# Kernel tuning notes

Measured on AMD Instinct MI355X. Metric: run time of the kernel, lower is better.

## Reference

```python
import jax, jax.numpy as jnp
import numpy as np

N_NODES = 100000
LEAKY_SLOPE = 0.01  # nn.LeakyReLU default

def setup_inputs() -> dict:
    key = jax.random.key(0)
    k1, k2, k3, k4, k5, k6 = jax.random.split(key, 6)
    in_dim, out_dim, ef_dim = 64, 64, 32
    E = 500000
    nf = jax.random.normal(k1, (N_NODES, in_dim), dtype=jnp.float32)
    ef = jax.random.normal(k2, (E, ef_dim), dtype=jnp.float32)
    src = jax.random.randint(k3, (E,), 0, N_NODES, dtype=jnp.int64 if jax.config.jax_enable_x64 else jnp.int32)
    dst = jax.random.randint(k4, (E,), 0, N_NODES, dtype=src.dtype)
    # torch Linear weights: (out, in), no bias
    We = jax.random.normal(k5, (out_dim, 2 * in_dim + ef_dim), dtype=jnp.float32) * 0.05
    Wn = jax.random.normal(k6, (out_dim, out_dim + in_dim), dtype=jnp.float32) * 0.05
    return {"nf": nf, "ef": ef, "src": src, "dst": dst, "We": We, "Wn": Wn}

def reference(nf, ef, src, dst, We, Wn):
    # Module adds reverse edges sharing the same edge features
    src_all = jnp.concatenate([src, dst])          # [2E]
    dst_all = jnp.concatenate([dst, src])          # [2E]
    ef_all = jnp.concatenate([ef, ef], axis=0)     # [2E, ef_dim]
    # message: concat(src_nf, dst_nf, ef) -> Linear -> LeakyReLU
    m_in = jnp.concatenate([nf[src_all], nf[dst_all], ef_all], axis=-1)  # [2E, 2*in+ef]
    msg = jax.nn.leaky_relu(m_in @ We.T, negative_slope=LEAKY_SLOPE)     # [2E, out]
    # reduce: sum messages at destination nodes
    red = jax.ops.segment_sum(msg, dst_all, num_segments=N_NODES)       # [N, out]
    # apply: concat(nf, red_msg) -> Linear -> LeakyReLU
    n_in = jnp.concatenate([nf, red], axis=-1)                          # [N, in+out]
    out_nf = jax.nn.leaky_relu(n_in @ Wn.T, negative_slope=LEAKY_SLOPE)
    return out_nf
```

## Files before the change

### kernel.cpp

```cpp
#include <hip/hip_runtime.h>
#include <stdint.h>


#define LEAKY(x) fmaxf((x), 0.01f * (x))
#define CAP 40
#define SCAT_BLOCKS 2048
typedef _Float16 f16;
typedef _Float16 h2 __attribute__((ext_vector_type(2)));
typedef int iv4 __attribute__((ext_vector_type(4)));

static __device__ __forceinline__ int swz(int k, int c) {
    return k * 128 + (c ^ (((k >> 2) & 7) << 2));
}

union H4 { f16 h[4]; h2 p[2]; short4 s; long long ll; };
union H8 { f16 h[8]; h2 p[4]; int4 q; };

__global__ void prep_weights_kernel(const float* __restrict__ We,
                                    const float* __restrict__ Wn,
                                    float* __restrict__ WTab,
                                    float* __restrict__ WTc,
                                    float* __restrict__ WTn,
                                    int* __restrict__ cnt, int N)
{
    const int stride = gridDim.x * blockDim.x;
    int i = blockIdx.x * blockDim.x + threadIdx.x;
    for (int j = i; j < 8192 + 2048 + 8192; j += stride) {
        if (j < 8192) {
            int k = j >> 7, n = j & 127;
            WTab[j] = We[(n & 63) * 160 + (n >> 6) * 64 + k];
        } else if (j < 10240) {
            int q = j - 8192; int k = q >> 6, n = q & 63;
            WTc[q] = We[n * 160 + 128 + k];
        } else {
            int q = j - 10240; int k = q >> 6, n = q & 63;
            WTn[q] = Wn[n * 128 + k];
        }
    }
    const int C4 = N * 4;
    for (int j = i; j < C4; j += stride) cnt[j] = 0;
}

static __device__ void scatter_body(int vb,
    const int* __restrict__ src, const int* __restrict__ dst,
    int* __restrict__ cnt, int2* __restrict__ inc, int E, int N)
{
    const int part = vb & 7;
    const int lo = (int)(((long long)N * part) >> 3);
    const int hi = (int)(((long long)N * (part + 1)) >> 3);
    const int tid = (vb >> 3) * 256 + threadIdx.x;
    const int tpp = (SCAT_BLOCKS >> 3) * 256;
    const int E4 = E >> 2;
    const iv4* src4 = (const iv4*)src;
    const iv4* dst4 = (const iv4*)dst;
    #define PUT(node, nbr, eid) \
        if ((node) >= lo && (node) < hi) { \
            const int p = atomicAdd(&cnt[(node) * 4], 1); \
            if (p < CAP) inc[(size_t)(node) * CAP + p] = make_int2((nbr) << 7, (eid) << 7); \
        }
    for (int j = tid; j < E4; j += tpp) {
        const iv4 s = __builtin_nontemporal_load(&src4[j]);
        const iv4 d = __builtin_nontemporal_load(&dst4[j]);
        const int e0 = 4 * j;
        PUT(d.x, s.x, e0 + 0)
        PUT(d.y, s.y, e0 + 1)
        PUT(d.z, s.z, e0 + 2)
        PUT(d.w, s.w, e0 + 3)
        PUT(s.x, d.x, e0 + 0)
        PUT(s.y, d.y, e0 + 1)
        PUT(s.z, d.z, e0 + 2)
        PUT(s.w, d.w, e0 + 3)
    }
    for (int i = (E4 << 2) + tid; i < E; i += tpp) {
        const int s = src[i], d = dst[i];
        PUT(d, s, i)
        PUT(s, d, i)
    }
    #undef PUT
}

static __device__ void gemm_c_body(float* lds, int bid,
    const float4* __restrict__ ef4, const float* __restrict__ WT,
    f16* __restrict__ C16, int M)
{
    float* As = lds;
    float* Ws = lds + 4096;
    const int t = threadIdx.x;
    const int tr = t >> 4, tc = t & 15;
    const int m0 = bid * 128;

    #pragma unroll
    for (int i = 0; i < 2; ++i)
        ((float4*)Ws)[t + 256 * i] = ((const float4*)WT)[t + 256 * i];
    #pragma unroll
    for (int i = 0; i < 4; ++i) {
        const int idx = t + 256 * i;
        const int m = idx >> 3, kq = idx & 7;
        float4 v = make_float4(0.f, 0.f, 0.f, 0.f);
        if (m0 + m < M) v = ef4[(size_t)(m0 + m) * 8 + kq];
        As[swz(4 * kq + 0, m)] = v.x;
        As[swz(4 * kq + 1, m)] = v.y;
        As[swz(4 * kq + 2, m)] = v.z;
        As[swz(4 * kq + 3, m)] = v.w;
    }
    __syncthreads();

    float acc[8][4];
    #pragma unroll
    for (int ri = 0; ri < 8; ++ri)
        #pragma unroll
        for (int ci = 0; ci < 4; ++ci) acc[ri][ci] = 0.f;

    #pragma unroll 8
    for (int k = 0; k < 32; ++k) {
        const float4 aLo = *(const float4*)&As[swz(k, tr * 4)];
        const float4 aHi = *(const float4*)&As[swz(k, 64 + tr * 4)];
        const float4 w  = *(const float4*)&Ws[k * 64 + tc * 4];
        const float av[8] = {aLo.x, aLo.y, aLo.z, aLo.w, aHi.x, aHi.y, aHi.z, aHi.w};
        const float bv[4] = {w.x, w.y, w.z, w.w};
        #pragma unroll
        for (int ri = 0; ri < 8; ++ri)
            #pragma unroll
            for (int ci = 0; ci < 4; ++ci) acc[ri][ci] += av[ri] * bv[ci];
    }

    #pragma unroll
    for (int ri = 0; ri < 8; ++ri) {
        const int v = m0 + ((ri < 4) ? (tr * 4 + ri) : (64 + tr * 4 + ri - 4));
        if (v < M) {
            H4 u;
            #pragma unroll
            for (int j = 0; j < 4; ++j) u.h[j] = (f16)acc[ri][j];
            *(short4*)&C16[(size_t)v * 64 + tc * 4] = u.s;
        }
    }
}

__global__ __launch_bounds__(256) void mega1_kernel(
    const int* __restrict__ src, const int* __restrict__ dst,
    int* __restrict__ cnt, int2* __restrict__ inc,
    const float4* __restrict__ ef4, const float* __restrict__ WTc,
    f16* __restrict__ C16, int E, int N)
{
    __shared__ float lds[6144];
    const int b = blockIdx.x;
    if (b < SCAT_BLOCKS) scatter_body(b, src, dst, cnt, inc, E, N);
    else                 gemm_c_body(lds, b - SCAT_BLOCKS, ef4, WTc, C16, E);
}

__global__ __launch_bounds__(256) void gemm_abp_kernel(
    const float4* __restrict__ nf4, const float* __restrict__ WTab,
    const float* __restrict__ WTn,
    f16* __restrict__ A16, f16* __restrict__ B16, f16* __restrict__ P16, int M)
{
    __shared__ float As[64 * 128];
    __shared__ float Wab[64 * 128];
    __shared__ float Wp[64 * 64];
    const int t = threadIdx.x;
    const int tr = t >> 4, tc = t & 15;
    const int m0 = blockIdx.x * 128;

    #pragma unroll
    for (int i = 0; i < 8; ++i)
        ((float4*)Wab)[t + 256 * i] = ((const float4*)WTab)[t + 256 * i];
    #pragma unroll
    for (int i = 0; i < 4; ++i)
        ((float4*)Wp)[t + 256 * i] = ((const float4*)WTn)[t + 256 * i];
    #pragma unroll
    for (int i = 0; i < 8; ++i) {
        const int idx = t + 256 * i;
        const int m = idx >> 4, kq = idx & 15;
        float4 v = make_float4(0.f, 0.f, 0.f, 0.f);
        if (m0 + m < M) v = nf4[(size_t)(m0 + m) * 16 + kq];
        As[swz(4 * kq + 0, m)] = v.x;
        As[swz(4 * kq + 1, m)] = v.y;
        As[swz(4 * kq + 2, m)] = v.z;
        As[swz(4 * kq + 3, m)] = v.w;
    }
    __syncthreads();

    float acc[8][8];
    float accp[8][4];
    #pragma unroll
    for (int ri = 0; ri < 8; ++ri) {
        #pragma unroll
        for (int ci = 0; ci < 8; ++ci) acc[ri][ci] = 0.f;
        #pragma unroll
        for (int ci = 0; ci < 4; ++ci) accp[ri][ci] = 0.f;
    }

    #pragma unroll 4
    for (int k = 0; k < 64; ++k) {
        const float4 aLo = *(const float4*)&As[swz(k, tr * 4)];
        const float4 aHi = *(const float4*)&As[swz(k, 64 + tr * 4)];
        const float4 bLo = *(const float4*)&Wab[k * 128 + tc * 4];
        const float4 bHi = *(const float4*)&Wab[k * 128 + 64 + tc * 4];
        const float4 w  = *(const float4*)&Wp[k * 64 + tc * 4];
        const float av[8] = {aLo.x, aLo.y, aLo.z, aLo.w, aHi.x, aHi.y, aHi.z, aHi.w};
        const float bv[8] = {bLo.x, bLo.y, bLo.z, bLo.w, bHi.x, bHi.y, bHi.z, bHi.w};
        const float wv[4] = {w.x, w.y, w.z, w.w};
        #pragma unroll
        for (int ri = 0; ri < 8; ++ri) {
            #pragma unroll
            for (int ci = 0; ci < 8; ++ci) acc[ri][ci] += av[ri] * bv[ci];
            #pragma unroll
            for (int ci = 0; ci < 4; ++ci) accp[ri][ci] += av[ri] * wv[ci];
        }
    }

    #pragma unroll
    for (int ri = 0; ri < 8; ++ri) {
        const int v = m0 + ((ri < 4) ? (tr * 4 + ri) : (64 + tr * 4 + ri - 4));
        if (v < M) {
            H4 lo, hi, pu;
            #pragma unroll
            for (int j = 0; j < 4; ++j) {
                lo.h[j] = (f16)acc[ri][j];
                hi.h[j] = (f16)acc[ri][4 + j];
                pu.h[j] = (f16)accp[ri][j];
            }
            *(short4*)&A16[(size_t)v * 64 + tc * 4] = lo.s;
            *(short4*)&B16[(size_t)v * 64 + tc * 4] = hi.s;
            *(short4*)&P16[(size_t)v * 64 + tc * 4] = pu.s;
        }
    }
}

__global__ __launch_bounds__(256, 4) void reduce_kernel(
    const f16* __restrict__ A16, const f16* __restrict__ B16,
    const f16* __restrict__ C16, const int* __restrict__ cnt,
    const int2* __restrict__ inc, f16* __restrict__ red16, int N)
{
    const int lane = threadIdx.x & 63;
    const int g = lane >> 3;
    const int sub = lane & 7;
    const int sub16 = sub * 16;
    const char* Ab = (const char*)A16;
    const char* Cb = (const char*)C16;
    const int part = blockIdx.x & 7;
    const int NO = (N + 7) >> 3;
    const int olo = (int)(((long long)NO * part) >> 3);
    const int ohi = (int)(((long long)NO * (part + 1)) >> 3);
    const int wid = (((blockIdx.x >> 3) * blockDim.x) + threadIdx.x) >> 6;
    const int wstride = ((gridDim.x >> 3) * blockDim.x) >> 6;
    const _Float16 k01 = (_Float16)0.01f;
    const h2 c001 = {k01, k01};
    for (int oct = olo + wid; oct < ohi; oct += wstride) {
        const int v = oct * 8 + g;
        const int vc = (v < N) ? v : (N - 1);
        const int len = min(cnt[vc * 4], CAP);
        const int ebase = vc * CAP;
        H8 bh; bh.q = *(const int4*)&B16[(size_t)vc * 64 + sub * 8];
        const h2 b0 = bh.p[0], b1 = bh.p[1], b2 = bh.p[2], b3 = bh.p[3];
        int mx = (len + 7) >> 3;
        mx = max(mx, __shfl_xor(mx, 8));
        mx = max(mx, __shfl_xor(mx, 16));
        mx = max(mx, __shfl_xor(mx, 32));
        float a0 = 0.f, a1 = 0.f, a2 = 0.f, a3 = 0.f;
        float a4 = 0.f, a5 = 0.f, a6 = 0.f, a7 = 0.f;
        for (int it = 0; it < mx; ++it) {
            const int el = it * 8;
            const int4 q0 = *(const int4*)&inc[ebase + el];
            const int4 q1 = *(const int4*)&inc[ebase + el + 2];
            const int4 q2 = *(const int4*)&inc[ebase + el + 4];
            const int4 q3 = *(const int4*)&inc[ebase + el + 6];
            float okf[8];
            unsigned ao[8], co[8];
            #pragma unroll
            for (int k2 = 0; k2 < 8; ++k2)
                okf[k2] = ((unsigned)(el + k2) < (unsigned)len) ? 1.0f : 0.0f;
            const int qa[8] = {q0.x, q0.z, q1.x, q1.z, q2.x, q2.z, q3.x, q3.z};
            const int qc[8] = {q0.y, q0.w, q1.y, q1.w, q2.y, q2.w, q3.y, q3.w};
            #pragma unroll
            for (int k2 = 0; k2 < 8; ++k2) {
                ao[k2] = (okf[k2] != 0.0f) ? (unsigned)qa[k2] : 0u;
                co[k2] = (okf[k2] != 0.0f) ? (unsigned)qc[k2] : 0u;
            }
            H8 Av[8], Cv[8];
            #pragma unroll
            for (int k2 = 0; k2 < 8; ++k2) {
                Av[k2].q = *(const int4*)(Ab + (size_t)ao[k2] + sub16);
                Cv[k2].q = *(const int4*)(Cb + (size_t)co[k2] + sub16);
            }
            #pragma unroll
            for (int k2 = 0; k2 < 8; ++k2) {
                h2 s0 = Av[k2].p[0] + Cv[k2].p[0] + b0;
                h2 s1 = Av[k2].p[1] + Cv[k2].p[1] + b1;
                h2 s2 = Av[k2].p[2] + Cv[k2].p[2] + b2;
                h2 s3 = Av[k2].p[3] + Cv[k2].p[3] + b3;
                s0 = __builtin_elementwise_max(s0, s0 * c001);
                s1 = __builtin_elementwise_max(s1, s1 * c001);
                s2 = __builtin_elementwise_max(s2, s2 * c001);
                s3 = __builtin_elementwise_max(s3, s3 * c001);
                a0 = fmaf((float)s0[0], okf[k2], a0);
                a1 = fmaf((float)s0[1], okf[k2], a1);
                a2 = fmaf((float)s1[0], okf[k2], a2);
                a3 = fmaf((float)s1[1], okf[k2], a3);
                a4 = fmaf((float)s2[0], okf[k2], a4);
                a5 = fmaf((float)s2[1], okf[k2], a5);
                a6 = fmaf((float)s3[0], okf[k2], a6);
                a7 = fmaf((float)s3[1], okf[k2], a7);
            }
        }
        if (v < N) {
            H8 u;
            u.h[0] = (f16)a0; u.h[1] = (f16)a1; u.h[2] = (f16)a2; u.h[3] = (f16)a3;
            u.h[4] = (f16)a4; u.h[5] = (f16)a5; u.h[6] = (f16)a6; u.h[7] = (f16)a7;
            *(int4*)&red16[(size_t)v * 64 + sub * 8] = u.q;
        }
    }
}

__global__ __launch_bounds__(256) void apply_lite_kernel(
    const f16* __restrict__ red16, const f16* __restrict__ P16,
    const float* __restrict__ WTn, float* __restrict__ out, int M)
{
    __shared__ float As[64 * 128];
    __shared__ float Ws[64 * 64];
    const int t = threadIdx.x;
    const int tr = t >> 4, tc = t & 15;
    const int m0 = blockIdx.x * 128;
    const float* WT1 = WTn + 4096;

    #pragma unroll
    for (int i = 0; i < 4; ++i)
        ((float4*)Ws)[t + 256 * i] = ((const float4*)WT1)[t + 256 * i];
    #pragma unroll
    for (int i = 0; i < 8; ++i) {
        const int idx = t + 256 * i;
        const int m = idx >> 4, kq = idx & 15;
        H4 v; v.ll = 0;
        if (m0 + m < M) v.s = *(const short4*)&red16[(size_t)(m0 + m) * 64 + kq * 4];
        As[swz(4 * kq + 0, m)] = (float)v.h[0];
        As[swz(4 * kq + 1, m)] = (float)v.h[1];
        As[swz(4 * kq + 2, m)] = (float)v.h[2];
        As[swz(4 * kq + 3, m)] = (float)v.h[3];
    }
    __syncthreads();

    float acc[8][4];
    #pragma unroll
    for (int ri = 0; ri < 8; ++ri)
        #pragma unroll
        for (int ci = 0; ci < 4; ++ci) acc[ri][ci] = 0.f;

    #pragma unroll 8
    for (int k = 0; k < 64; ++k) {
        const float4 aLo = *(const float4*)&As[swz(k, tr * 4)];
        const float4 aHi = *(const float4*)&As[swz(k, 64 + tr * 4)];
        const float4 w  = *(const float4*)&Ws[k * 64 + tc * 4];
        const float av[8] = {aLo.x, aLo.y, aLo.z, aLo.w, aHi.x, aHi.y, aHi.z, aHi.w};
        const float bv[4] = {w.x, w.y, w.z, w.w};
        #pragma unroll
        for (int ri = 0; ri < 8; ++ri)
            #pragma unroll
            for (int ci = 0; ci < 4; ++ci) acc[ri][ci] += av[ri] * bv[ci];
    }

    #pragma unroll
    for (int ri = 0; ri < 8; ++ri) {
        const int v = m0 + ((ri < 4) ? (tr * 4 + ri) : (64 + tr * 4 + ri - 4));
        if (v < M) {
            H4 pv; pv.s = *(const short4*)&P16[(size_t)v * 64 + tc * 4];
            float4 o;
            o.x = LEAKY(acc[ri][0] + (float)pv.h[0]);
            o.y = LEAKY(acc[ri][1] + (float)pv.h[1]);
            o.z = LEAKY(acc[ri][2] + (float)pv.h[2]);
            o.w = LEAKY(acc[ri][3] + (float)pv.h[3]);
            *(float4*)&out[(size_t)v * 64 + tc * 4] = o;
        }
    }
}

extern "C" void kernel_launch(void* const* d_in, const int* in_sizes, int n_in,
                              void* d_out, int out_size, void* d_ws, size_t ws_size,
                              hipStream_t stream) {
    const float* nf  = (const float*)d_in[0];
    const float* ef  = (const float*)d_in[1];
    const int*   src = (const int*)d_in[2];
    const int*   dst = (const int*)d_in[3];
    const float* We  = (const float*)d_in[4];
    const float* Wn  = (const float*)d_in[5];

    const int N = in_sizes[0] / 64;
    const int E = in_sizes[2];

    char* p = (char*)d_ws;
    auto alloc = [&](size_t bytes) -> char* {
        char* r = p; p += (bytes + 255) & ~(size_t)255; return r;
    };
    f16*   red16 = (f16*)alloc((size_t)N * 64 * 2);
    float* WTab  = (float*)alloc(8192 * 4);
    float* WTc   = (float*)alloc(2048 * 4);
    float* WTn   = (float*)alloc(8192 * 4);
    int2*  inc   = (int2*)alloc((size_t)N * CAP * 8);
    int*   cnt   = (int*)alloc((size_t)N * 4 * 4);
    f16*   A16   = (f16*)alloc((size_t)N * 64 * 2);
    f16*   B16   = (f16*)alloc((size_t)N * 64 * 2);
    f16*   C16   = (f16*)alloc((size_t)E * 64 * 2);
    f16*   P16   = (f16*)alloc((size_t)N * 64 * 2);

    const int nC = (E + 127) >> 7;
    const int nAB = (N + 127) >> 7;
    const int NO = (N + 7) >> 3;
    const int redBlocks = (((NO + 3) / 4) + 7) & ~7;

    prep_weights_kernel<<<512, 256, 0, stream>>>(We, Wn, WTab, WTc, WTn, cnt, N);
    mega1_kernel<<<SCAT_BLOCKS + nC, 256, 0, stream>>>(src, dst, cnt, inc,
                                                       (const float4*)ef, WTc, C16, E, N);
    gemm_abp_kernel<<<nAB, 256, 0, stream>>>((const float4*)nf, WTab, WTn,
                                             A16, B16, P16, N);
    reduce_kernel<<<redBlocks, 256, 0, stream>>>(A16, B16, C16, cnt, inc, red16, N);
    apply_lite_kernel<<<(N + 127) / 128, 256, 0, stream>>>(red16, P16, WTn, (float*)d_out, N);
}
```

Measured before the change: 288.6 us.

## Fuse node apply GEMM into reduce kernel and halve scatter blocks

```diff
diff --git a/kernel.cpp b/kernel.cpp
--- a/kernel.cpp
+++ b/kernel.cpp
@@ -4,7 +4,7 @@
 
 #define LEAKY(x) fmaxf((x), 0.01f * (x))
 #define CAP 40
-#define SCAT_BLOCKS 2048
+#define SCAT_BLOCKS 1024
 typedef _Float16 f16;
 typedef _Float16 h2 __attribute__((ext_vector_type(2)));
 typedef int iv4 __attribute__((ext_vector_type(4)));
@@ -229,12 +229,23 @@
 __global__ __launch_bounds__(256, 4) void reduce_kernel(
     const f16* __restrict__ A16, const f16* __restrict__ B16,
     const f16* __restrict__ C16, const int* __restrict__ cnt,
-    const int2* __restrict__ inc, f16* __restrict__ red16, int N)
-{
+    const int2* __restrict__ inc, const f16* __restrict__ P16,
+    const float* __restrict__ WTn, float* __restrict__ outp, int N)
+{
+    __shared__ float W1[64 * 64];
+    {
+        const float4* wsrc = (const float4*)(WTn + 4096);
+        #pragma unroll
+        for (int i = 0; i < 4; ++i)
+            ((float4*)W1)[threadIdx.x + 256 * i] = wsrc[threadIdx.x + 256 * i];
+    }
+    __syncthreads();
+
     const int lane = threadIdx.x & 63;
     const int g = lane >> 3;
     const int sub = lane & 7;
     const int sub16 = sub * 16;
+    const int gbase = lane & 56;
     const char* Ab = (const char*)A16;
     const char* Cb = (const char*)C16;
     const int part = blockIdx.x & 7;
@@ -256,8 +267,7 @@
         mx = max(mx, __shfl_xor(mx, 8));
         mx = max(mx, __shfl_xor(mx, 16));
         mx = max(mx, __shfl_xor(mx, 32));
-        float a0 = 0.f, a1 = 0.f, a2 = 0.f, a3 = 0.f;
-        float a4 = 0.f, a5 = 0.f, a6 = 0.f, a7 = 0.f;
+        float areg[8] = {0.f, 0.f, 0.f, 0.f, 0.f, 0.f, 0.f, 0.f};
         for (int it = 0; it < mx; ++it) {
             const int el = it * 8;
             const int4 q0 = *(const int4*)&inc[ebase + el];
@@ -292,82 +302,44 @@
                 s1 = __builtin_elementwise_max(s1, s1 * c001);
                 s2 = __builtin_elementwise_max(s2, s2 * c001);
                 s3 = __builtin_elementwise_max(s3, s3 * c001);
-                a0 = fmaf((float)s0[0], okf[k2], a0);
-                a1 = fmaf((float)s0[1], okf[k2], a1);
-                a2 = fmaf((float)s1[0], okf[k2], a2);
-                a3 = fmaf((float)s1[1], okf[k2], a3);
-                a4 = fmaf((float)s2[0], okf[k2], a4);
-                a5 = fmaf((float)s2[1], okf[k2], a5);
-                a6 = fmaf((float)s3[0], okf[k2], a6);
-                a7 = fmaf((float)s3[1], okf[k2], a7);
+                areg[0] = fmaf((float)s0[0], okf[k2], areg[0]);
+                areg[1] = fmaf((float)s0[1], okf[k2], areg[1]);
+                areg[2] = fmaf((float)s1[0], okf[k2], areg[2]);
+                areg[3] = fmaf((float)s1[1], okf[k2], areg[3]);
+                areg[4] = fmaf((float)s2[0], okf[k2], areg[4]);
+                areg[5] = fmaf((float)s2[1], okf[k2], areg[5]);
+                areg[6] = fmaf((float)s3[0], okf[k2], areg[6]);
+                areg[7] = fmaf((float)s3[1], okf[k2], areg[7]);
+            }
+        }
+        H8 pv; pv.q = *(const int4*)&P16[(size_t)vc * 64 + sub * 8];
+        float o[8];
+        #pragma unroll
+        for (int j = 0; j < 8; ++j) o[j] = (float)pv.h[j];
+        #pragma unroll
+        for (int r = 0; r < 8; ++r) {
+            const float av = areg[r];
+            #pragma unroll
+            for (int s = 0; s < 8; ++s) {
+                const int k = s * 8 + r;
+                const float rk = __shfl(av, gbase + s, 64);
+                const float4 w0 = *(const float4*)&W1[k * 64 + sub * 8];
+                const float4 w1 = *(const float4*)&W1[k * 64 + sub * 8 + 4];
+                o[0] = fmaf(rk, w0.x, o[0]);
+                o[1] = fmaf(rk, w0.y, o[1]);
+                o[2] = fmaf(rk, w0.z, o[2]);
+                o[3] = fmaf(rk, w0.w, o[3]);
+                o[4] = fmaf(rk, w1.x, o[4]);
+                o[5] = fmaf(rk, w1.y, o[5]);
+                o[6] = fmaf(rk, w1.z, o[6]);
+                o[7] = fmaf(rk, w1.w, o[7]);
             }
         }
         if (v < N) {
-            H8 u;
-            u.h[0] = (f16)a0; u.h[1] = (f16)a1; u.h[2] = (f16)a2; u.h[3] = (f16)a3;
-            u.h[4] = (f16)a4; u.h[5] = (f16)a5; u.h[6] = (f16)a6; u.h[7] = (f16)a7;
-            *(int4*)&red16[(size_t)v * 64 + sub * 8] = u.q;
-        }
-    }
-}
-
-__global__ __launch_bounds__(256) void apply_lite_kernel(
-    const f16* __restrict__ red16, const f16* __restrict__ P16,
-    const float* __restrict__ WTn, float* __restrict__ out, int M)
-{
-    __shared__ float As[64 * 128];
-    __shared__ float Ws[64 * 64];
-    const int t = threadIdx.x;
-    const int tr = t >> 4, tc = t & 15;
-    const int m0 = blockIdx.x * 128;
-    const float* WT1 = WTn + 4096;
-
-    #pragma unroll
-    for (int i = 0; i < 4; ++i)
-        ((float4*)Ws)[t + 256 * i] = ((const float4*)WT1)[t + 256 * i];
-    #pragma unroll
-    for (int i = 0; i < 8; ++i) {
-        const int idx = t + 256 * i;
-        const int m = idx >> 4, kq = idx & 15;
-        H4 v; v.ll = 0;
-        if (m0 + m < M) v.s = *(const short4*)&red16[(size_t)(m0 + m) * 64 + kq * 4];
-        As[swz(4 * kq + 0, m)] = (float)v.h[0];
-        As[swz(4 * kq + 1, m)] = (float)v.h[1];
-        As[swz(4 * kq + 2, m)] = (float)v.h[2];
-        As[swz(4 * kq + 3, m)] = (float)v.h[3];
-    }
-    __syncthreads();
-
-    float acc[8][4];
-    #pragma unroll
-    for (int ri = 0; ri < 8; ++ri)
-        #pragma unroll
-        for (int ci = 0; ci < 4; ++ci) acc[ri][ci] = 0.f;
-
-    #pragma unroll 8
-    for (int k = 0; k < 64; ++k) {
-        const float4 aLo = *(const float4*)&As[swz(k, tr * 4)];
-        const float4 aHi = *(const float4*)&As[swz(k, 64 + tr * 4)];
-        const float4 w  = *(const float4*)&Ws[k * 64 + tc * 4];
-        const float av[8] = {aLo.x, aLo.y, aLo.z, aLo.w, aHi.x, aHi.y, aHi.z, aHi.w};
-        const float bv[4] = {w.x, w.y, w.z, w.w};
-        #pragma unroll
-        for (int ri = 0; ri < 8; ++ri)
-            #pragma unroll
-            for (int ci = 0; ci < 4; ++ci) acc[ri][ci] += av[ri] * bv[ci];
-    }
-
-    #pragma unroll
-    for (int ri = 0; ri < 8; ++ri) {
-        const int v = m0 + ((ri < 4) ? (tr * 4 + ri) : (64 + tr * 4 + ri - 4));
-        if (v < M) {
-            H4 pv; pv.s = *(const short4*)&P16[(size_t)v * 64 + tc * 4];
-            float4 o;
-            o.x = LEAKY(acc[ri][0] + (float)pv.h[0]);
-            o.y = LEAKY(acc[ri][1] + (float)pv.h[1]);
-            o.z = LEAKY(acc[ri][2] + (float)pv.h[2]);
-            o.w = LEAKY(acc[ri][3] + (float)pv.h[3]);
-            *(float4*)&out[(size_t)v * 64 + tc * 4] = o;
+            float4 s0 = make_float4(LEAKY(o[0]), LEAKY(o[1]), LEAKY(o[2]), LEAKY(o[3]));
+            float4 s1 = make_float4(LEAKY(o[4]), LEAKY(o[5]), LEAKY(o[6]), LEAKY(o[7]));
+            *(float4*)&outp[(size_t)v * 64 + sub * 8] = s0;
+            *(float4*)&outp[(size_t)v * 64 + sub * 8 + 4] = s1;
         }
     }
 }
@@ -389,7 +361,6 @@
     auto alloc = [&](size_t bytes) -> char* {
         char* r = p; p += (bytes + 255) & ~(size_t)255; return r;
     };
-    f16*   red16 = (f16*)alloc((size_t)N * 64 * 2);
     float* WTab  = (float*)alloc(8192 * 4);
     float* WTc   = (float*)alloc(2048 * 4);
     float* WTn   = (float*)alloc(8192 * 4);
@@ -410,6 +381,6 @@
                                                        (const float4*)ef, WTc, C16, E, N);
     gemm_abp_kernel<<<nAB, 256, 0, stream>>>((const float4*)nf, WTab, WTn,
                                              A16, B16, P16, N);
-    reduce_kernel<<<redBlocks, 256, 0, stream>>>(A16, B16, C16, cnt, inc, red16, N);
-    apply_lite_kernel<<<(N + 127) / 128, 256, 0, stream>>>(red16, P16, WTn, (float*)d_out, N);
-}
+    reduce_kernel<<<redBlocks, 256, 0, stream>>>(A16, B16, C16, cnt, inc,
+                                                 P16, WTn, (float*)d_out, N);
+}
```

New measurement: 293.9 us. Within noise of the previous version (+1.8%).
